# Performance work log

Measured on AMD Instinct MI355X. Metric: run time of the kernel, lower is better.

## Reference

```python
import jax, jax.numpy as jnp
import numpy as np

# int64 needed: the torch module hashes with int64 primes (2654435761 > 2**31)
jax.config.update("jax_enable_x64", True)

NUM_LEVELS = 16
BASE_RES = 16
MAX_RES = 2048
LOG2_HASHMAP = 19
FEATURE_DIM = 2
HASHMAP_SIZE = 2 ** LOG2_HASHMAP
N_POINTS = 1_048_576

_growth = np.exp((np.log(MAX_RES) - np.log(BASE_RES)) / (NUM_LEVELS - 1))
RESOLUTIONS = [min(int(BASE_RES * _growth ** l), MAX_RES) for l in range(NUM_LEVELS)]
PRIMES = np.array([1, 2654435761, 805459861], dtype=np.int64)
# corner order matches torch triple loop: index c = i*4 + j*2 + k -> offset [i, j, k]
OFFSETS = np.array([[i, j, k] for i in range(2) for j in range(2) for k in range(2)],
                   dtype=np.int64)  # (8, 3)


def setup_inputs() -> dict:
    key = jax.random.key(0)
    k1, k2 = jax.random.split(key)
    positions = jax.random.uniform(k1, (N_POINTS, 3), dtype=jnp.float32) * 2.0 - 1.0  # in [-1, 1]
    hash_table = jax.random.normal(k2, (HASHMAP_SIZE, FEATURE_DIM), dtype=jnp.float32) * 1e-4
    return {"positions": positions, "hash_table": hash_table}


def _encode(positions, hash_table):
    p = (positions + 1.0) * 0.5  # map [-1,1] -> [0,1]
    primes = jnp.asarray(PRIMES)
    offs = jnp.asarray(OFFSETS)           # (8, 3) int64
    offs_f = offs.astype(p.dtype)         # (8, 3)
    feats = []
    for res in RESOLUTIONS:
        sp = p * (res - 1)                # (N, 3)
        gp = jnp.floor(sp)
        w = sp - gp                       # fractional weights (N, 3)
        corners = gp.astype(jnp.int64)[:, None, :] + offs[None]   # (N, 8, 3)
        corners = jnp.clip(corners, 0, res - 1)
        h = (corners[..., 0] * primes[0]) ^ (corners[..., 1] * primes[1]) ^ (corners[..., 2] * primes[2])
        idx = h % HASHMAP_SIZE            # (N, 8)
        cf = hash_table[idx]              # gather: (N, 8, F)
        # trilinear weights: prod over dims of (w if offset bit else 1-w)
        wcomp = offs_f[None] * w[:, None, :] + (1.0 - offs_f[None]) * (1.0 - w[:, None, :])  # (N,8,3)
        tw = wcomp[..., 0] * wcomp[..., 1] * wcomp[..., 2]        # (N, 8)
        feats.append(jnp.einsum('nc,ncf->nf', tw, cf))            # (N, F)
    return jnp.concatenate(feats, axis=-1)  # (N, NUM_LEVELS * F)


def reference(positions, hash_table):
    return _encode(positions, hash_table)
```

## Files before the change

### kernel.cpp

```cpp
#include <hip/hip_runtime.h>
#include <cstdint>

#define P2 2654435761u
#define P3 805459861u
#define HMASK 524287u

typedef float nfloat4 __attribute__((ext_vector_type(4)));
typedef float nfloat2 __attribute__((ext_vector_type(2)));

__constant__ int RES[16] = {16, 22, 30, 42, 58, 80, 111, 153,
                            212, 294, 406, 561, 776, 1072, 1482, 2048};

__global__ __launch_bounds__(256) void hash_enc_kernel(
    const float* __restrict__ pos, const float2* __restrict__ tbl,
    float2* __restrict__ out, int n)
{
    const float4* __restrict__ tbl4 = (const float4*)tbl;

    __shared__ int sres[16];
    __shared__ float spos[48];

    const int tid = threadIdx.x;
    if (tid < 16) sres[tid] = RES[tid];

    const int p0 = blockIdx.x * 16;
    if (p0 + 16 <= n) {
        if (tid < 12) {
            nfloat4 v = __builtin_nontemporal_load(
                (const nfloat4*)(pos + (size_t)p0 * 3) + tid);
            ((nfloat4*)spos)[tid] = v;
        }
    } else {
        if (tid < 48) {
            int gi = p0 * 3 + tid;
            spos[tid] = (gi < 3 * n) ? pos[gi] : 0.0f;
        }
    }
    __syncthreads();

    const int t = blockIdx.x * 256 + tid;
    const int i = t >> 4;
    const int l = t & 15;
    if (i >= n) return;
    const int li = tid >> 4;

    float x = (spos[3 * li + 0] + 1.0f) * 0.5f;
    float y = (spos[3 * li + 1] + 1.0f) * 0.5f;
    float z = (spos[3 * li + 2] + 1.0f) * 0.5f;

    const int rm1 = sres[l] - 1;
    const float rf = (float)rm1;

    float sx = x * rf, sy = y * rf, sz = z * rf;
    float fx = floorf(sx), fy = floorf(sy), fz = floorf(sz);
    float wx = sx - fx, wy = sy - fy, wz = sz - fz;
    int x0 = (int)fx, y0 = (int)fy, z0 = (int)fz;
    int x0c = min(max(x0, 0), rm1), x1c = min(max(x0 + 1, 0), rm1);
    int y0c = min(max(y0, 0), rm1), y1c = min(max(y0 + 1, 0), rm1);
    int z0c = min(max(z0, 0), rm1), z1c = min(max(z0 + 1, 0), rm1);

    uint32_t hy0 = (uint32_t)y0c * P2, hy1 = (uint32_t)y1c * P2;
    uint32_t hz0 = (uint32_t)z0c * P3, hz1 = (uint32_t)z1c * P3;
    uint32_t m00 = hy0 ^ hz0;
    uint32_t m01 = hy0 ^ hz1;
    uint32_t m10 = hy1 ^ hz0;
    uint32_t m11 = hy1 ^ hz1;

    uint32_t hx0 = (uint32_t)x0c;
    uint32_t j000 = (hx0 ^ m00) & HMASK;
    uint32_t j001 = (hx0 ^ m01) & HMASK;
    uint32_t j010 = (hx0 ^ m10) & HMASK;
    uint32_t j011 = (hx0 ^ m11) & HMASK;

    float4 q00 = tbl4[j000 >> 1];
    float4 q01 = tbl4[j001 >> 1];
    float4 q10 = tbl4[j010 >> 1];
    float4 q11 = tbl4[j011 >> 1];

    float2 c000, c001, c010, c011, c100, c101, c110, c111;
    bool b00 = (j000 & 1), b01 = (j001 & 1), b10 = (j010 & 1), b11 = (j011 & 1);
    c000 = b00 ? make_float2(q00.z, q00.w) : make_float2(q00.x, q00.y);
    c100 = b00 ? make_float2(q00.x, q00.y) : make_float2(q00.z, q00.w);
    c001 = b01 ? make_float2(q01.z, q01.w) : make_float2(q01.x, q01.y);
    c101 = b01 ? make_float2(q01.x, q01.y) : make_float2(q01.z, q01.w);
    c010 = b10 ? make_float2(q10.z, q10.w) : make_float2(q10.x, q10.y);
    c110 = b10 ? make_float2(q10.x, q10.y) : make_float2(q10.z, q10.w);
    c011 = b11 ? make_float2(q11.z, q11.w) : make_float2(q11.x, q11.y);
    c111 = b11 ? make_float2(q11.x, q11.y) : make_float2(q11.z, q11.w);

    if (x0c & 1) {
        uint32_t hx1 = (uint32_t)x1c;
        c100 = tbl[(hx1 ^ m00) & HMASK];
        c101 = tbl[(hx1 ^ m01) & HMASK];
        c110 = tbl[(hx1 ^ m10) & HMASK];
        c111 = tbl[(hx1 ^ m11) & HMASK];
    }

    float ux = 1.0f - wx, uy = 1.0f - wy, uz = 1.0f - wz;
    float w00 = ux * uy, w01 = ux * wy, w10 = wx * uy, w11 = wx * wy;
    float f0, f1;
    f0  = (w00 * uz) * c000.x; f1  = (w00 * uz) * c000.y;
    f0 += (w00 * wz) * c001.x; f1 += (w00 * wz) * c001.y;
    f0 += (w01 * uz) * c010.x; f1 += (w01 * uz) * c010.y;
    f0 += (w01 * wz) * c011.x; f1 += (w01 * wz) * c011.y;
    f0 += (w10 * uz) * c100.x; f1 += (w10 * uz) * c100.y;
    f0 += (w10 * wz) * c101.x; f1 += (w10 * wz) * c101.y;
    f0 += (w11 * uz) * c110.x; f1 += (w11 * uz) * c110.y;
    f0 += (w11 * wz) * c111.x; f1 += (w11 * wz) * c111.y;

    nfloat2 r; r.x = f0; r.y = f1;
    __builtin_nontemporal_store(r, (nfloat2*)&out[t]);
}

extern "C" void kernel_launch(void* const* d_in, const int* in_sizes, int n_in,
                              void* d_out, int out_size, void* d_ws, size_t ws_size,
                              hipStream_t stream) {
    const float* pos = (const float*)d_in[0];
    const float2* tbl = (const float2*)d_in[1];
    float2* out = (float2*)d_out;
    int n = in_sizes[0] / 3;
    long long total = (long long)n * 16;
    dim3 grid((unsigned)((total + 255) / 256)), block(256);
    hash_enc_kernel<<<grid, block, 0, stream>>>(pos, tbl, out, n);
}
```

Before: 525.6 us.

## Precompute paired-corner tables for x0^x1 of 3 and 7 to cut gathers

```diff
diff --git a/kernel.cpp b/kernel.cpp
--- a/kernel.cpp
+++ b/kernel.cpp
@@ -4,6 +4,7 @@
 #define P2 2654435761u
 #define P3 805459861u
 #define HMASK 524287u
+#define HSIZE 524288
 
 typedef float nfloat4 __attribute__((ext_vector_type(4)));
 typedef float nfloat2 __attribute__((ext_vector_type(2)));
@@ -11,9 +12,22 @@
 __constant__ int RES[16] = {16, 22, 30, 42, 58, 80, 111, 153,
                             212, 294, 406, 561, 776, 1072, 1482, 2048};
 
+__global__ __launch_bounds__(256) void build_pairs(
+    const float2* __restrict__ tbl, float4* __restrict__ T3,
+    float4* __restrict__ T7)
+{
+    int j = blockIdx.x * 256 + threadIdx.x;
+    float2 a  = tbl[j];
+    float2 b3 = tbl[j ^ 3];
+    float2 b7 = tbl[j ^ 7];
+    T3[j] = make_float4(a.x, a.y, b3.x, b3.y);
+    T7[j] = make_float4(a.x, a.y, b7.x, b7.y);
+}
+
 __global__ __launch_bounds__(256) void hash_enc_kernel(
     const float* __restrict__ pos, const float2* __restrict__ tbl,
-    float2* __restrict__ out, int n)
+    const float4* __restrict__ T3, const float4* __restrict__ T7,
+    float2* __restrict__ out, int n, int useT)
 {
     const float4* __restrict__ tbl4 = (const float4*)tbl;
 
@@ -72,13 +86,29 @@
     uint32_t j010 = (hx0 ^ m10) & HMASK;
     uint32_t j011 = (hx0 ^ m11) & HMASK;
 
-    float4 q00 = tbl4[j000 >> 1];
-    float4 q01 = tbl4[j001 >> 1];
-    float4 q10 = tbl4[j010 >> 1];
-    float4 q11 = tbl4[j011 >> 1];
+    uint32_t m = (uint32_t)(x0c ^ x1c);
+    bool t3 = useT && (m == 3);
+    bool t7 = useT && (m == 7);
+    bool t37 = t3 | t7;
+    bool covered = (m == 1) | t37;
+
+    const float4* bp = t3 ? T3 : (t7 ? T7 : tbl4);
+    uint32_t k00 = t37 ? j000 : (j000 >> 1);
+    uint32_t k01 = t37 ? j001 : (j001 >> 1);
+    uint32_t k10 = t37 ? j010 : (j010 >> 1);
+    uint32_t k11 = t37 ? j011 : (j011 >> 1);
+
+    float4 q00 = bp[k00];
+    float4 q01 = bp[k01];
+    float4 q10 = bp[k10];
+    float4 q11 = bp[k11];
+
+    bool b00 = !t37 && (j000 & 1);
+    bool b01 = !t37 && (j001 & 1);
+    bool b10 = !t37 && (j010 & 1);
+    bool b11 = !t37 && (j011 & 1);
 
     float2 c000, c001, c010, c011, c100, c101, c110, c111;
-    bool b00 = (j000 & 1), b01 = (j001 & 1), b10 = (j010 & 1), b11 = (j011 & 1);
     c000 = b00 ? make_float2(q00.z, q00.w) : make_float2(q00.x, q00.y);
     c100 = b00 ? make_float2(q00.x, q00.y) : make_float2(q00.z, q00.w);
     c001 = b01 ? make_float2(q01.z, q01.w) : make_float2(q01.x, q01.y);
@@ -88,7 +118,7 @@
     c011 = b11 ? make_float2(q11.z, q11.w) : make_float2(q11.x, q11.y);
     c111 = b11 ? make_float2(q11.x, q11.y) : make_float2(q11.z, q11.w);
 
-    if (x0c & 1) {
+    if (!covered) {
         uint32_t hx1 = (uint32_t)x1c;
         c100 = tbl[(hx1 ^ m00) & HMASK];
         c101 = tbl[(hx1 ^ m01) & HMASK];
@@ -119,7 +149,15 @@
     const float2* tbl = (const float2*)d_in[1];
     float2* out = (float2*)d_out;
     int n = in_sizes[0] / 3;
+
+    int useT = (ws_size >= (size_t)(16u << 20)) ? 1 : 0;
+    float4* T3 = (float4*)d_ws;
+    float4* T7 = T3 + HSIZE;
+    if (useT) {
+        build_pairs<<<dim3(HSIZE / 256), dim3(256), 0, stream>>>(tbl, T3, T7);
+    }
+
     long long total = (long long)n * 16;
     dim3 grid((unsigned)((total + 255) / 256)), block(256);
-    hash_enc_kernel<<<grid, block, 0, stream>>>(pos, tbl, out, n);
+    hash_enc_kernel<<<grid, block, 0, stream>>>(pos, tbl, T3, T7, out, n, useT);
 }
```

Result: slower. 738.7 us (+40.5%).

## Materialize dense grids for coarse levels and use nontemporal hash-table loads

Applied to the files above, without the earlier changes.

```diff
diff --git a/kernel.cpp b/kernel.cpp
--- a/kernel.cpp
+++ b/kernel.cpp
@@ -7,15 +7,43 @@
 
 typedef float nfloat4 __attribute__((ext_vector_type(4)));
 typedef float nfloat2 __attribute__((ext_vector_type(2)));
+typedef nfloat4 uf4 __attribute__((aligned(8)));
 
 __constant__ int RES[16] = {16, 22, 30, 42, 58, 80, 111, 153,
                             212, 294, 406, 561, 776, 1072, 1482, 2048};
 
+#define D_N0 4096
+#define D_N1 10648
+#define D_N2 27000
+#define D_N3 74088
+#define D_O0 0
+#define D_O1 4096
+#define D_O2 14744
+#define D_O3 41744
+#define D_TOTAL 115832
+
+__global__ __launch_bounds__(256) void build_dense(
+    const float2* __restrict__ tbl, float2* __restrict__ D)
+{
+    int idx = blockIdx.x * 256 + threadIdx.x;
+    if (idx >= D_TOTAL) return;
+    int r, base;
+    if (idx < D_O1)      { r = 16; base = D_O0; }
+    else if (idx < D_O2) { r = 22; base = D_O1; }
+    else if (idx < D_O3) { r = 30; base = D_O2; }
+    else                 { r = 42; base = D_O3; }
+    int k = idx - base;
+    int z = k % r; int xy = k / r;
+    int y = xy % r; int x = xy / r;
+    uint32_t h = ((uint32_t)x ^ (uint32_t)y * P2 ^ (uint32_t)z * P3) & HMASK;
+    D[idx] = tbl[h];
+}
+
 __global__ __launch_bounds__(256) void hash_enc_kernel(
     const float* __restrict__ pos, const float2* __restrict__ tbl,
-    float2* __restrict__ out, int n)
+    const float2* __restrict__ D, float2* __restrict__ out, int n, int useD)
 {
-    const float4* __restrict__ tbl4 = (const float4*)tbl;
+    const nfloat4* __restrict__ tbl4 = (const nfloat4*)tbl;
 
     __shared__ int sres[16];
     __shared__ float spos[48];
@@ -48,7 +76,8 @@
     float y = (spos[3 * li + 1] + 1.0f) * 0.5f;
     float z = (spos[3 * li + 2] + 1.0f) * 0.5f;
 
-    const int rm1 = sres[l] - 1;
+    const int r = sres[l];
+    const int rm1 = r - 1;
     const float rf = (float)rm1;
 
     float sx = x * rf, sy = y * rf, sz = z * rf;
@@ -59,41 +88,66 @@
     int y0c = min(max(y0, 0), rm1), y1c = min(max(y0 + 1, 0), rm1);
     int z0c = min(max(z0, 0), rm1), z1c = min(max(z0 + 1, 0), rm1);
 
-    uint32_t hy0 = (uint32_t)y0c * P2, hy1 = (uint32_t)y1c * P2;
-    uint32_t hz0 = (uint32_t)z0c * P3, hz1 = (uint32_t)z1c * P3;
-    uint32_t m00 = hy0 ^ hz0;
-    uint32_t m01 = hy0 ^ hz1;
-    uint32_t m10 = hy1 ^ hz0;
-    uint32_t m11 = hy1 ^ hz1;
+    float2 c000, c001, c010, c011, c100, c101, c110, c111;
 
-    uint32_t hx0 = (uint32_t)x0c;
-    uint32_t j000 = (hx0 ^ m00) & HMASK;
-    uint32_t j001 = (hx0 ^ m01) & HMASK;
-    uint32_t j010 = (hx0 ^ m10) & HMASK;
-    uint32_t j011 = (hx0 ^ m11) & HMASK;
+    if (useD && l < 4) {
+        const int dbase = (l == 0) ? D_O0 : (l == 1) ? D_O1
+                        : (l == 2) ? D_O2 : D_O3;
+        const float2* __restrict__ Dl = D + dbase;
+        int i00 = (x0c * r + y0c) * r + z0c;
+        int i01 = (x0c * r + y1c) * r + z0c;
+        int i10 = (x1c * r + y0c) * r + z0c;
+        int i11 = (x1c * r + y1c) * r + z0c;
+        nfloat4 q00 = *(const uf4*)(Dl + i00);
+        nfloat4 q01 = *(const uf4*)(Dl + i01);
+        nfloat4 q10 = *(const uf4*)(Dl + i10);
+        nfloat4 q11 = *(const uf4*)(Dl + i11);
+        c000 = make_float2(q00.x, q00.y); c001 = make_float2(q00.z, q00.w);
+        c010 = make_float2(q01.x, q01.y); c011 = make_float2(q01.z, q01.w);
+        c100 = make_float2(q10.x, q10.y); c101 = make_float2(q10.z, q10.w);
+        c110 = make_float2(q11.x, q11.y); c111 = make_float2(q11.z, q11.w);
+    } else {
+        uint32_t hy0 = (uint32_t)y0c * P2, hy1 = (uint32_t)y1c * P2;
+        uint32_t hz0 = (uint32_t)z0c * P3, hz1 = (uint32_t)z1c * P3;
+        uint32_t m00 = hy0 ^ hz0;
+        uint32_t m01 = hy0 ^ hz1;
+        uint32_t m10 = hy1 ^ hz0;
+        uint32_t m11 = hy1 ^ hz1;
 
-    float4 q00 = tbl4[j000 >> 1];
-    float4 q01 = tbl4[j001 >> 1];
-    float4 q10 = tbl4[j010 >> 1];
-    float4 q11 = tbl4[j011 >> 1];
+        uint32_t hx0 = (uint32_t)x0c;
+        uint32_t j000 = (hx0 ^ m00) & HMASK;
+        uint32_t j001 = (hx0 ^ m01) & HMASK;
+        uint32_t j010 = (hx0 ^ m10) & HMASK;
+        uint32_t j011 = (hx0 ^ m11) & HMASK;
 
-    float2 c000, c001, c010, c011, c100, c101, c110, c111;
-    bool b00 = (j000 & 1), b01 = (j001 & 1), b10 = (j010 & 1), b11 = (j011 & 1);
-    c000 = b00 ? make_float2(q00.z, q00.w) : make_float2(q00.x, q00.y);
-    c100 = b00 ? make_float2(q00.x, q00.y) : make_float2(q00.z, q00.w);
-    c001 = b01 ? make_float2(q01.z, q01.w) : make_float2(q01.x, q01.y);
-    c101 = b01 ? make_float2(q01.x, q01.y) : make_float2(q01.z, q01.w);
-    c010 = b10 ? make_float2(q10.z, q10.w) : make_float2(q10.x, q10.y);
-    c110 = b10 ? make_float2(q10.x, q10.y) : make_float2(q10.z, q10.w);
-    c011 = b11 ? make_float2(q11.z, q11.w) : make_float2(q11.x, q11.y);
-    c111 = b11 ? make_float2(q11.x, q11.y) : make_float2(q11.z, q11.w);
+        nfloat4 q00 = __builtin_nontemporal_load(tbl4 + (j000 >> 1));
+        nfloat4 q01 = __builtin_nontemporal_load(tbl4 + (j001 >> 1));
+        nfloat4 q10 = __builtin_nontemporal_load(tbl4 + (j010 >> 1));
+        nfloat4 q11 = __builtin_nontemporal_load(tbl4 + (j011 >> 1));
 
-    if (x0c & 1) {
-        uint32_t hx1 = (uint32_t)x1c;
-        c100 = tbl[(hx1 ^ m00) & HMASK];
-        c101 = tbl[(hx1 ^ m01) & HMASK];
-        c110 = tbl[(hx1 ^ m10) & HMASK];
-        c111 = tbl[(hx1 ^ m11) & HMASK];
+        bool b00 = (j000 & 1), b01 = (j001 & 1);
+        bool b10 = (j010 & 1), b11 = (j011 & 1);
+        c000 = b00 ? make_float2(q00.z, q00.w) : make_float2(q00.x, q00.y);
+        c100 = b00 ? make_float2(q00.x, q00.y) : make_float2(q00.z, q00.w);
+        c001 = b01 ? make_float2(q01.z, q01.w) : make_float2(q01.x, q01.y);
+        c101 = b01 ? make_float2(q01.x, q01.y) : make_float2(q01.z, q01.w);
+        c010 = b10 ? make_float2(q10.z, q10.w) : make_float2(q10.x, q10.y);
+        c110 = b10 ? make_float2(q10.x, q10.y) : make_float2(q10.z, q10.w);
+        c011 = b11 ? make_float2(q11.z, q11.w) : make_float2(q11.x, q11.y);
+        c111 = b11 ? make_float2(q11.x, q11.y) : make_float2(q11.z, q11.w);
+
+        if (x0c & 1) {
+            uint32_t hx1 = (uint32_t)x1c;
+            const nfloat2* t2 = (const nfloat2*)tbl;
+            nfloat2 a = __builtin_nontemporal_load(t2 + ((hx1 ^ m00) & HMASK));
+            nfloat2 b = __builtin_nontemporal_load(t2 + ((hx1 ^ m01) & HMASK));
+            nfloat2 c = __builtin_nontemporal_load(t2 + ((hx1 ^ m10) & HMASK));
+            nfloat2 d = __builtin_nontemporal_load(t2 + ((hx1 ^ m11) & HMASK));
+            c100 = make_float2(a.x, a.y);
+            c101 = make_float2(b.x, b.y);
+            c110 = make_float2(c.x, c.y);
+            c111 = make_float2(d.x, d.y);
+        }
     }
 
     float ux = 1.0f - wx, uy = 1.0f - wy, uz = 1.0f - wz;
@@ -108,8 +162,8 @@
     f0 += (w11 * uz) * c110.x; f1 += (w11 * uz) * c110.y;
     f0 += (w11 * wz) * c111.x; f1 += (w11 * wz) * c111.y;
 
-    nfloat2 r; r.x = f0; r.y = f1;
-    __builtin_nontemporal_store(r, (nfloat2*)&out[t]);
+    nfloat2 rr; rr.x = f0; rr.y = f1;
+    __builtin_nontemporal_store(rr, (nfloat2*)&out[t]);
 }
 
 extern "C" void kernel_launch(void* const* d_in, const int* in_sizes, int n_in,
@@ -119,7 +173,14 @@
     const float2* tbl = (const float2*)d_in[1];
     float2* out = (float2*)d_out;
     int n = in_sizes[0] / 3;
+
+    int useD = (ws_size >= (size_t)(D_TOTAL * sizeof(float2))) ? 1 : 0;
+    float2* D = (float2*)d_ws;
+    if (useD) {
+        build_dense<<<dim3((D_TOTAL + 255) / 256), dim3(256), 0, stream>>>(tbl, D);
+    }
+
     long long total = (long long)n * 16;
     dim3 grid((unsigned)((total + 255) / 256)), block(256);
-    hash_enc_kernel<<<grid, block, 0, stream>>>(pos, tbl, out, n);
+    hash_enc_kernel<<<grid, block, 0, stream>>>(pos, tbl, D, out, n, useD);
 }
```

Result: slower. 884.0 us (+68.2%).

## Bucket-sort points spatially before hash encoding to improve table gather locality

Applied to the files above, without the earlier changes.

```diff
diff --git a/kernel.cpp b/kernel.cpp
--- a/kernel.cpp
+++ b/kernel.cpp
@@ -4,6 +4,7 @@
 #define P2 2654435761u
 #define P3 805459861u
 #define HMASK 524287u
+#define NBUCK 32768
 
 typedef float nfloat4 __attribute__((ext_vector_type(4)));
 typedef float nfloat2 __attribute__((ext_vector_type(2)));
@@ -11,105 +12,163 @@
 __constant__ int RES[16] = {16, 22, 30, 42, 58, 80, 111, 153,
                             212, 294, 406, 561, 776, 1072, 1482, 2048};
 
-__global__ __launch_bounds__(256) void hash_enc_kernel(
+__device__ __forceinline__ int bucket_of(float px, float py, float pz) {
+    int bx = min(31, max(0, (int)((px + 1.0f) * 16.0f)));
+    int by = min(31, max(0, (int)((py + 1.0f) * 16.0f)));
+    int bz = min(31, max(0, (int)((pz + 1.0f) * 16.0f)));
+    return (bx * 32 + by) * 32 + bz;
+}
+
+__global__ __launch_bounds__(256) void zero_counts(int* c) {
+    int i = blockIdx.x * 256 + threadIdx.x;
+    if (i < NBUCK) c[i] = 0;
+}
+
+__global__ __launch_bounds__(256) void count_kernel(
+    const float* __restrict__ pos, int* __restrict__ counts, int n) {
+    int i = blockIdx.x * 256 + threadIdx.x;
+    if (i >= n) return;
+    atomicAdd(&counts[bucket_of(pos[3*i], pos[3*i+1], pos[3*i+2])], 1);
+}
+
+__global__ __launch_bounds__(1024) void scan_kernel(int* counts) {
+    __shared__ int part[1024];
+    int t = threadIdx.x;
+    int base = t * 32;
+    int s = 0;
+    #pragma unroll
+    for (int j = 0; j < 32; ++j) s += counts[base + j];
+    part[t] = s;
+    __syncthreads();
+    int orig = s;
+    for (int off = 1; off < 1024; off <<= 1) {
+        int v = (t >= off) ? part[t - off] : 0;
+        __syncthreads();
+        part[t] += v;
+        __syncthreads();
+    }
+    int run = part[t] - orig;
+    for (int j = 0; j < 32; ++j) {
+        int c = counts[base + j];
+        counts[base + j] = run;
+        run += c;
+    }
+}
+
+__global__ __launch_bounds__(256) void scatter_kernel(
+    const float* __restrict__ pos, int* __restrict__ counts,
+    int* __restrict__ perm, int n) {
+    int i = blockIdx.x * 256 + threadIdx.x;
+    if (i >= n) return;
+    int b = bucket_of(pos[3*i], pos[3*i+1], pos[3*i+2]);
+    int slot = atomicAdd(&counts[b], 1);
+    perm[slot] = i;
+}
+
+__global__ __launch_bounds__(256) void hash_enc_sorted(
     const float* __restrict__ pos, const float2* __restrict__ tbl,
-    float2* __restrict__ out, int n)
+    float2* __restrict__ out, const int* __restrict__ perm,
+    int n, int usePerm)
 {
     const float4* __restrict__ tbl4 = (const float4*)tbl;
 
-    __shared__ int sres[16];
-    __shared__ float spos[48];
+    __shared__ int   sidx[64];
+    __shared__ float sx[64], sy[64], sz[64];
+    __shared__ float2 sout[64][17];
 
     const int tid = threadIdx.x;
-    if (tid < 16) sres[tid] = RES[tid];
+    const int base = blockIdx.x * 64;
 
-    const int p0 = blockIdx.x * 16;
-    if (p0 + 16 <= n) {
-        if (tid < 12) {
-            nfloat4 v = __builtin_nontemporal_load(
-                (const nfloat4*)(pos + (size_t)p0 * 3) + tid);
-            ((nfloat4*)spos)[tid] = v;
-        }
-    } else {
-        if (tid < 48) {
-            int gi = p0 * 3 + tid;
-            spos[tid] = (gi < 3 * n) ? pos[gi] : 0.0f;
-        }
+    if (tid < 64) {
+        int gi = base + tid;
+        int pi = 0;
+        if (gi < n) pi = usePerm ? perm[gi] : gi;
+        sidx[tid] = pi;
+        float px = pos[3*pi+0], py = pos[3*pi+1], pz = pos[3*pi+2];
+        sx[tid] = (px + 1.0f) * 0.5f;
+        sy[tid] = (py + 1.0f) * 0.5f;
+        sz[tid] = (pz + 1.0f) * 0.5f;
     }
     __syncthreads();
 
-    const int t = blockIdx.x * 256 + tid;
-    const int i = t >> 4;
-    const int l = t & 15;
-    if (i >= n) return;
-    const int li = tid >> 4;
+    const int wave = tid >> 6, lane = tid & 63;
+    const float x = sx[lane], y = sy[lane], z = sz[lane];
 
-    float x = (spos[3 * li + 0] + 1.0f) * 0.5f;
-    float y = (spos[3 * li + 1] + 1.0f) * 0.5f;
-    float z = (spos[3 * li + 2] + 1.0f) * 0.5f;
+    #pragma unroll
+    for (int s = 0; s < 4; ++s) {
+        const int l = wave + 4 * s;
+        const int rm1 = RES[l] - 1;
+        const float rf = (float)rm1;
 
-    const int rm1 = sres[l] - 1;
-    const float rf = (float)rm1;
+        float sxf = x * rf, syf = y * rf, szf = z * rf;
+        float fx = floorf(sxf), fy = floorf(syf), fz = floorf(szf);
+        float wx = sxf - fx, wy = syf - fy, wz = szf - fz;
+        int x0 = (int)fx, y0 = (int)fy, z0 = (int)fz;
+        int x0c = min(max(x0, 0), rm1), x1c = min(max(x0 + 1, 0), rm1);
+        int y0c = min(max(y0, 0), rm1), y1c = min(max(y0 + 1, 0), rm1);
+        int z0c = min(max(z0, 0), rm1), z1c = min(max(z0 + 1, 0), rm1);
 
-    float sx = x * rf, sy = y * rf, sz = z * rf;
-    float fx = floorf(sx), fy = floorf(sy), fz = floorf(sz);
-    float wx = sx - fx, wy = sy - fy, wz = sz - fz;
-    int x0 = (int)fx, y0 = (int)fy, z0 = (int)fz;
-    int x0c = min(max(x0, 0), rm1), x1c = min(max(x0 + 1, 0), rm1);
-    int y0c = min(max(y0, 0), rm1), y1c = min(max(y0 + 1, 0), rm1);
-    int z0c = min(max(z0, 0), rm1), z1c = min(max(z0 + 1, 0), rm1);
+        uint32_t hy0 = (uint32_t)y0c * P2, hy1 = (uint32_t)y1c * P2;
+        uint32_t hz0 = (uint32_t)z0c * P3, hz1 = (uint32_t)z1c * P3;
+        uint32_t m00 = hy0 ^ hz0, m01 = hy0 ^ hz1;
+        uint32_t m10 = hy1 ^ hz0, m11 = hy1 ^ hz1;
 
-    uint32_t hy0 = (uint32_t)y0c * P2, hy1 = (uint32_t)y1c * P2;
-    uint32_t hz0 = (uint32_t)z0c * P3, hz1 = (uint32_t)z1c * P3;
-    uint32_t m00 = hy0 ^ hz0;
-    uint32_t m01 = hy0 ^ hz1;
-    uint32_t m10 = hy1 ^ hz0;
-    uint32_t m11 = hy1 ^ hz1;
+        uint32_t hx0 = (uint32_t)x0c;
+        uint32_t j000 = (hx0 ^ m00) & HMASK;
+        uint32_t j001 = (hx0 ^ m01) & HMASK;
+        uint32_t j010 = (hx0 ^ m10) & HMASK;
+        uint32_t j011 = (hx0 ^ m11) & HMASK;
 
-    uint32_t hx0 = (uint32_t)x0c;
-    uint32_t j000 = (hx0 ^ m00) & HMASK;
-    uint32_t j001 = (hx0 ^ m01) & HMASK;
-    uint32_t j010 = (hx0 ^ m10) & HMASK;
-    uint32_t j011 = (hx0 ^ m11) & HMASK;
+        float4 q00 = tbl4[j000 >> 1];
+        float4 q01 = tbl4[j001 >> 1];
+        float4 q10 = tbl4[j010 >> 1];
+        float4 q11 = tbl4[j011 >> 1];
 
-    float4 q00 = tbl4[j000 >> 1];
-    float4 q01 = tbl4[j001 >> 1];
-    float4 q10 = tbl4[j010 >> 1];
-    float4 q11 = tbl4[j011 >> 1];
+        bool b00 = (j000 & 1), b01 = (j001 & 1);
+        bool b10 = (j010 & 1), b11 = (j011 & 1);
+        float2 c000 = b00 ? make_float2(q00.z, q00.w) : make_float2(q00.x, q00.y);
+        float2 c100 = b00 ? make_float2(q00.x, q00.y) : make_float2(q00.z, q00.w);
+        float2 c001 = b01 ? make_float2(q01.z, q01.w) : make_float2(q01.x, q01.y);
+        float2 c101 = b01 ? make_float2(q01.x, q01.y) : make_float2(q01.z, q01.w);
+        float2 c010 = b10 ? make_float2(q10.z, q10.w) : make_float2(q10.x, q10.y);
+        float2 c110 = b10 ? make_float2(q10.x, q10.y) : make_float2(q10.z, q10.w);
+        float2 c011 = b11 ? make_float2(q11.z, q11.w) : make_float2(q11.x, q11.y);
+        float2 c111 = b11 ? make_float2(q11.x, q11.y) : make_float2(q11.z, q11.w);
 
-    float2 c000, c001, c010, c011, c100, c101, c110, c111;
-    bool b00 = (j000 & 1), b01 = (j001 & 1), b10 = (j010 & 1), b11 = (j011 & 1);
-    c000 = b00 ? make_float2(q00.z, q00.w) : make_float2(q00.x, q00.y);
-    c100 = b00 ? make_float2(q00.x, q00.y) : make_float2(q00.z, q00.w);
-    c001 = b01 ? make_float2(q01.z, q01.w) : make_float2(q01.x, q01.y);
-    c101 = b01 ? make_float2(q01.x, q01.y) : make_float2(q01.z, q01.w);
-    c010 = b10 ? make_float2(q10.z, q10.w) : make_float2(q10.x, q10.y);
-    c110 = b10 ? make_float2(q10.x, q10.y) : make_float2(q10.z, q10.w);
-    c011 = b11 ? make_float2(q11.z, q11.w) : make_float2(q11.x, q11.y);
-    c111 = b11 ? make_float2(q11.x, q11.y) : make_float2(q11.z, q11.w);
+        if (x0c & 1) {
+            uint32_t hx1 = (uint32_t)x1c;
+            c100 = tbl[(hx1 ^ m00) & HMASK];
+            c101 = tbl[(hx1 ^ m01) & HMASK];
+            c110 = tbl[(hx1 ^ m10) & HMASK];
+            c111 = tbl[(hx1 ^ m11) & HMASK];
+        }
 
-    if (x0c & 1) {
-        uint32_t hx1 = (uint32_t)x1c;
-        c100 = tbl[(hx1 ^ m00) & HMASK];
-        c101 = tbl[(hx1 ^ m01) & HMASK];
-        c110 = tbl[(hx1 ^ m10) & HMASK];
-        c111 = tbl[(hx1 ^ m11) & HMASK];
+        float ux = 1.0f - wx, uy = 1.0f - wy, uz = 1.0f - wz;
+        float w00 = ux * uy, w01 = ux * wy, w10 = wx * uy, w11 = wx * wy;
+        float f0, f1;
+        f0  = (w00 * uz) * c000.x; f1  = (w00 * uz) * c000.y;
+        f0 += (w00 * wz) * c001.x; f1 += (w00 * wz) * c001.y;
+        f0 += (w01 * uz) * c010.x; f1 += (w01 * uz) * c010.y;
+        f0 += (w01 * wz) * c011.x; f1 += (w01 * wz) * c011.y;
+        f0 += (w10 * uz) * c100.x; f1 += (w10 * uz) * c100.y;
+        f0 += (w10 * wz) * c101.x; f1 += (w10 * wz) * c101.y;
+        f0 += (w11 * uz) * c110.x; f1 += (w11 * uz) * c110.y;
+        f0 += (w11 * wz) * c111.x; f1 += (w11 * wz) * c111.y;
+
+        sout[lane][l] = make_float2(f0, f1);
     }
+    __syncthreads();
 
-    float ux = 1.0f - wx, uy = 1.0f - wy, uz = 1.0f - wz;
-    float w00 = ux * uy, w01 = ux * wy, w10 = wx * uy, w11 = wx * wy;
-    float f0, f1;
-    f0  = (w00 * uz) * c000.x; f1  = (w00 * uz) * c000.y;
-    f0 += (w00 * wz) * c001.x; f1 += (w00 * wz) * c001.y;
-    f0 += (w01 * uz) * c010.x; f1 += (w01 * uz) * c010.y;
-    f0 += (w01 * wz) * c011.x; f1 += (w01 * wz) * c011.y;
-    f0 += (w10 * uz) * c100.x; f1 += (w10 * uz) * c100.y;
-    f0 += (w10 * wz) * c101.x; f1 += (w10 * wz) * c101.y;
-    f0 += (w11 * uz) * c110.x; f1 += (w11 * uz) * c110.y;
-    f0 += (w11 * wz) * c111.x; f1 += (w11 * wz) * c111.y;
-
-    nfloat2 r; r.x = f0; r.y = f1;
-    __builtin_nontemporal_store(r, (nfloat2*)&out[t]);
+    int q = tid >> 2, part = tid & 3;
+    if (base + q < n) {
+        int oi = sidx[q] * 16 + part * 4;
+        float2 a = sout[q][part*4+0], b = sout[q][part*4+1];
+        float2 c = sout[q][part*4+2], d = sout[q][part*4+3];
+        nfloat4 v0; v0.x = a.x; v0.y = a.y; v0.z = b.x; v0.w = b.y;
+        nfloat4 v1; v1.x = c.x; v1.y = c.y; v1.z = d.x; v1.w = d.y;
+        __builtin_nontemporal_store(v0, (nfloat4*)&out[oi]);
+        __builtin_nontemporal_store(v1, (nfloat4*)&out[oi + 2]);
+    }
 }
 
 extern "C" void kernel_launch(void* const* d_in, const int* in_sizes, int n_in,
@@ -119,7 +178,19 @@
     const float2* tbl = (const float2*)d_in[1];
     float2* out = (float2*)d_out;
     int n = in_sizes[0] / 3;
-    long long total = (long long)n * 16;
-    dim3 grid((unsigned)((total + 255) / 256)), block(256);
-    hash_enc_kernel<<<grid, block, 0, stream>>>(pos, tbl, out, n);
+
+    size_t need = (size_t)NBUCK * 4 + (size_t)n * 4;
+    int usePerm = (ws_size >= need) ? 1 : 0;
+    int* counts = (int*)d_ws;
+    int* perm = counts + NBUCK;
+
+    if (usePerm) {
+        zero_counts<<<dim3((NBUCK + 255) / 256), dim3(256), 0, stream>>>(counts);
+        count_kernel<<<dim3((n + 255) / 256), dim3(256), 0, stream>>>(pos, counts, n);
+        scan_kernel<<<dim3(1), dim3(1024), 0, stream>>>(counts);
+        scatter_kernel<<<dim3((n + 255) / 256), dim3(256), 0, stream>>>(pos, counts, perm, n);
+    }
+
+    hash_enc_sorted<<<dim3((n + 63) / 64), dim3(256), 0, stream>>>(
+        pos, tbl, out, perm, n, usePerm);
 }
```

Result: no change. 521.5 us (-0.8%).
